# Kernel tuning notes

Hardware: AMD Instinct MI355X
Metric: run time of the kernel (lower is better)

The kernel has to match this reference:

```python
import jax, jax.numpy as jnp
import numpy as np

EPS = 1e-8


def setup_inputs() -> dict:
    key = jax.random.key(0)
    k1, k2, k3, k4 = jax.random.split(key, 4)
    N, E, d = 10000, 5000, 128
    F = jax.random.normal(k1, (N, d), dtype=jnp.float32)
    H = jax.random.uniform(k2, (N, E), dtype=jnp.float32)
    Dv = jax.random.uniform(k3, (N, N), dtype=jnp.float32)
    De = jax.random.uniform(k4, (E, E), dtype=jnp.float32)
    return {"F": F, "H": H, "Dv": Dv, "De": De}


def reference(F, H, Dv, De):
    # Only the diagonals of Dv/De are used by the original (torch.diag extraction).
    dv = jnp.diagonal(Dv)                      # [N]
    de = jnp.diagonal(De)                      # [E]
    dv_inv_sqrt = (dv + EPS) ** -0.5           # diag of Dv^{-1/2}
    de_inv = 1.0 / (de + EPS)                  # diag of De^{-1}
    # L = I - Dv^{-1/2} H De^{-1} H^T Dv^{-1/2}
    # trace(F^T L F) = ||F||_F^2 - sum_e de_inv[e] * ||(H^T (Dv^{-1/2} F))[e]||^2
    Fs = F * dv_inv_sqrt[:, None]              # [N, d]
    M = H.T @ Fs                               # [E, d]
    trace_term = jnp.sum(F * F) - jnp.sum(de_inv[:, None] * (M * M))
    # use_rayleigh=False; reduction='mean' -> divide by N
    loss = trace_term / F.shape[0]
    return loss
```

## Files before the change

### kernel.cpp

```cpp
#include <hip/hip_runtime.h>

#define EPSF 1e-8f

typedef __attribute__((ext_vector_type(8))) short bf16x8;
typedef __attribute__((ext_vector_type(4))) float f32x4;

constexpr int Nv     = 10000;
constexpr int Ne     = 5000;
constexpr int Dd     = 128;
constexpr int NPAD   = 10016;
constexpr int EPAD   = 5120;
constexpr int KSTEPS = 313;
constexpr int KSPLIT = 16;
constexpr int STEPS_PER = (KSTEPS + KSPLIT - 1) / KSPLIT;

__device__ __forceinline__ unsigned short f2bf_rne(float f) {
    unsigned int u = __builtin_bit_cast(unsigned int, f);
    u += 0x7fffu + ((u >> 16) & 1u);
    return (unsigned short)(u >> 16);
}

__global__ void prep_de_kernel(const float* __restrict__ De, float* __restrict__ de_inv) {
    int e = blockIdx.x * 256 + threadIdx.x;
    if (e < EPAD) de_inv[e] = (e < Ne) ? 1.0f / (De[(size_t)e * (Ne + 1)] + EPSF) : 0.0f;
}

__global__ void prep_fst_kernel(const float* __restrict__ F, const float* __restrict__ Dv,
                                short* __restrict__ Fst) {
    int n = blockIdx.x * 256 + threadIdx.x;
    int c = blockIdx.y;
    if (n < NPAD) {
        unsigned short b = 0;
        if (n < Nv) {
            float s = 1.0f / sqrtf(Dv[(size_t)n * (Nv + 1)] + EPSF);
            b = f2bf_rne(F[(size_t)n * Dd + c] * s);
        }
        Fst[(size_t)c * NPAD + n] = (short)b;
    }
}

__global__ void sum_ff_kernel(const float* __restrict__ F, float* __restrict__ out0) {
    const float4* F4 = (const float4*)F;
    int base = blockIdx.x * 512 + threadIdx.x;
    float4 a = F4[base];
    float4 b = F4[base + 256];
    float sum = a.x*a.x + a.y*a.y + a.z*a.z + a.w*a.w
              + b.x*b.x + b.y*b.y + b.z*b.z + b.w*b.w;
    #pragma unroll
    for (int off = 32; off; off >>= 1) sum += __shfl_down(sum, off);
    if ((threadIdx.x & 63) == 0) atomicAdd(out0, sum);
}

__global__ __launch_bounds__(256, 2)
void gemm_split_kernel(const float* __restrict__ H, const short* __restrict__ Fst,
                       float* __restrict__ M) {
    __shared__ unsigned int Alds[128 * 20];

    const int t  = threadIdx.x;
    const int w  = t >> 6;
    const int l  = t & 63;
    const int lm = l & 15;
    const int q  = l >> 4;
    const int e0 = blockIdx.x * 128;
    const int sb = blockIdx.y * STEPS_PER;
    const int se = min(sb + STEPS_PER, KSTEPS);

    const int rp  = t & 15;
    const int cp4 = t >> 4;

    f32x4 acc[2][8];
    #pragma unroll
    for (int a = 0; a < 2; ++a)
        #pragma unroll
        for (int b = 0; b < 8; ++b) acc[a][b] = (f32x4){0.f, 0.f, 0.f, 0.f};

    for (int s = sb; s < se; ++s) {
        const int n0 = s * 32;

        bf16x8 Bf[8];
        #pragma unroll
        for (int cb = 0; cb < 8; ++cb) {
            const int c = cb * 16 + lm;
            Bf[cb] = *(const bf16x8*)(Fst + (size_t)c * NPAD + n0 + q * 8);
        }

        const int n  = n0 + 2 * rp;
        const bool vn = (n < Nv);
        #pragma unroll
        for (int j = 0; j < 4; ++j) {
            const int cp = cp4 + 16 * j;
            const int el = 2 * cp;
            const int e  = e0 + el;
            float2 a0 = make_float2(0.f, 0.f), a1 = make_float2(0.f, 0.f);
            if (vn && e < Ne) {
                a0 = *(const float2*)(H + (size_t)n * Ne + e);
                a1 = *(const float2*)(H + (size_t)(n + 1) * Ne + e);
            }
            unsigned int w0 = (unsigned int)f2bf_rne(a0.x) | ((unsigned int)f2bf_rne(a1.x) << 16);
            unsigned int w1 = (unsigned int)f2bf_rne(a0.y) | ((unsigned int)f2bf_rne(a1.y) << 16);
            Alds[el * 20 + rp]       = w0;
            Alds[(el + 1) * 20 + rp] = w1;
        }
        __syncthreads();

        bf16x8 Af[2];
        #pragma unroll
        for (int eb = 0; eb < 2; ++eb) {
            const int el = (2 * w + eb) * 16 + lm;
            Af[eb] = *(const bf16x8*)((const char*)Alds + el * 80 + q * 16);
        }
        __syncthreads();

        #pragma unroll
        for (int cb = 0; cb < 8; ++cb)
            #pragma unroll
            for (int eb = 0; eb < 2; ++eb)
                acc[eb][cb] = __builtin_amdgcn_mfma_f32_16x16x32_bf16(
                    Af[eb], Bf[cb], acc[eb][cb], 0, 0, 0);
    }

    #pragma unroll
    for (int eb = 0; eb < 2; ++eb) {
        #pragma unroll
        for (int cb = 0; cb < 8; ++cb) {
            const int c = cb * 16 + lm;
            #pragma unroll
            for (int r = 0; r < 4; ++r) {
                const int el = (2 * w + eb) * 16 + q * 4 + r;
                atomicAdd(&M[(size_t)(e0 + el) * 128 + c], acc[eb][cb][r]);
            }
        }
    }
}

__global__ void reduce_m_kernel(const float* __restrict__ M, const float* __restrict__ de_inv,
                                float* __restrict__ outS) {
    const float4* M4 = (const float4*)M;
    int base = blockIdx.x * 512 + threadIdx.x;
    float sum = 0.f;
    #pragma unroll
    for (int i = 0; i < 2; ++i) {
        int idx = base + i * 256;
        float4 m = M4[idx];
        float wgt = de_inv[idx >> 5];
        sum += wgt * (m.x*m.x + m.y*m.y + m.z*m.z + m.w*m.w);
    }
    #pragma unroll
    for (int off = 32; off; off >>= 1) sum += __shfl_down(sum, off);
    if ((threadIdx.x & 63) == 0) atomicAdd(outS, sum);
}

__global__ void final_kernel(const float* __restrict__ ws0, float* __restrict__ out) {
    out[0] = (ws0[0] - ws0[1]) * (1.0f / (float)Nv);
}

extern "C" void kernel_launch(void* const* d_in, const int* in_sizes, int n_in,
                              void* d_out, int out_size, void* d_ws, size_t ws_size,
                              hipStream_t stream) {
    (void)in_sizes; (void)n_in; (void)out_size; (void)ws_size;
    const float* F  = (const float*)d_in[0];
    const float* H  = (const float*)d_in[1];
    const float* Dv = (const float*)d_in[2];
    const float* De = (const float*)d_in[3];
    float* out = (float*)d_out;

    float* ws0    = (float*)d_ws;
    float* M      = ws0 + 16;
    float* de_inv = M + (size_t)EPAD * 128;
    short* Fst    = (short*)(de_inv + EPAD);

    hipMemsetAsync(d_ws, 0, 64 + (size_t)EPAD * 128 * 4, stream);

    prep_de_kernel <<<EPAD / 256, 256, 0, stream>>>(De, de_inv);
    prep_fst_kernel<<<dim3((NPAD + 255) / 256, 128), 256, 0, stream>>>(F, Dv, Fst);
    sum_ff_kernel  <<<625, 256, 0, stream>>>(F, ws0);
    gemm_split_kernel<<<dim3(EPAD / 128, KSPLIT), 256, 0, stream>>>(H, Fst, M);
    reduce_m_kernel<<<320, 256, 0, stream>>>(M, de_inv, ws0 + 1);
    final_kernel   <<<1, 1, 0, stream>>>(ws0, out);
}
```

Measured before the change: 709.5 us.

## Restructure GEMM to per-wave 32x32 MFMA tiles with split-K partial buffers

The shared-memory-staged block GEMM is replaced by independent waves. Each wave owns a 32-column slice of H and accumulates all 128 feature columns with 32x32x16 bf16 MFMAs, reading H directly from global memory with a one-step register prefetch. The float atomics into M are replaced by plain stores into per-split partial buffers, which the reduce kernel sums and weights, so M no longer needs a large memset. The diagonal extraction is precomputed once and the sum of F squared is folded into the prep kernel. The per-lane H loads are strided by row (a single float per row), which risks poorer coalescing than before, and the partial buffers add extra memory traffic.

After: 964.3 us. +35.9%, slower.

```diff
diff --git a/kernel.cpp b/kernel.cpp
--- a/kernel.cpp
+++ b/kernel.cpp
@@ -3,16 +3,16 @@
 #define EPSF 1e-8f
 
 typedef __attribute__((ext_vector_type(8))) short bf16x8;
-typedef __attribute__((ext_vector_type(4))) float f32x4;
+typedef __attribute__((ext_vector_type(16))) float f32x16;
 
 constexpr int Nv     = 10000;
 constexpr int Ne     = 5000;
 constexpr int Dd     = 128;
 constexpr int NPAD   = 10016;
-constexpr int EPAD   = 5120;
-constexpr int KSTEPS = 313;
+constexpr int NT16   = 626;
+constexpr int ETILES = 157;
+constexpr int EW     = ETILES * 32;
 constexpr int KSPLIT = 16;
-constexpr int STEPS_PER = (KSTEPS + KSPLIT - 1) / KSPLIT;
 
 __device__ __forceinline__ unsigned short f2bf_rne(float f) {
     unsigned int u = __builtin_bit_cast(unsigned int, f);
@@ -20,131 +20,106 @@
     return (unsigned short)(u >> 16);
 }
 
-__global__ void prep_de_kernel(const float* __restrict__ De, float* __restrict__ de_inv) {
-    int e = blockIdx.x * 256 + threadIdx.x;
-    if (e < EPAD) de_inv[e] = (e < Ne) ? 1.0f / (De[(size_t)e * (Ne + 1)] + EPSF) : 0.0f;
+__global__ void prep_diag_kernel(const float* __restrict__ Dv, const float* __restrict__ De,
+                                 float* __restrict__ dvis, float* __restrict__ de_inv) {
+    int i = blockIdx.x * 256 + threadIdx.x;
+    if (i < NPAD) dvis[i] = (i < Nv) ? rsqrtf(Dv[(size_t)i * (Nv + 1)] + EPSF) : 0.0f;
+    if (i < EW)   de_inv[i] = (i < Ne) ? 1.0f / (De[(size_t)i * (Ne + 1)] + EPSF) : 0.0f;
 }
 
-__global__ void prep_fst_kernel(const float* __restrict__ F, const float* __restrict__ Dv,
-                                short* __restrict__ Fst) {
+__global__ void prep_fst_kernel(const float* __restrict__ F, const float* __restrict__ dvis,
+                                short* __restrict__ Fst, float* __restrict__ out0) {
     int n = blockIdx.x * 256 + threadIdx.x;
     int c = blockIdx.y;
+    float v = 0.0f;
     if (n < NPAD) {
         unsigned short b = 0;
-        if (n < Nv) {
-            float s = 1.0f / sqrtf(Dv[(size_t)n * (Nv + 1)] + EPSF);
-            b = f2bf_rne(F[(size_t)n * Dd + c] * s);
-        }
+        if (n < Nv) { v = F[(size_t)n * Dd + c]; b = f2bf_rne(v * dvis[n]); }
         Fst[(size_t)c * NPAD + n] = (short)b;
     }
-}
-
-__global__ void sum_ff_kernel(const float* __restrict__ F, float* __restrict__ out0) {
-    const float4* F4 = (const float4*)F;
-    int base = blockIdx.x * 512 + threadIdx.x;
-    float4 a = F4[base];
-    float4 b = F4[base + 256];
-    float sum = a.x*a.x + a.y*a.y + a.z*a.z + a.w*a.w
-              + b.x*b.x + b.y*b.y + b.z*b.z + b.w*b.w;
+    float sum = v * v;
     #pragma unroll
     for (int off = 32; off; off >>= 1) sum += __shfl_down(sum, off);
     if ((threadIdx.x & 63) == 0) atomicAdd(out0, sum);
 }
 
-__global__ __launch_bounds__(256, 2)
-void gemm_split_kernel(const float* __restrict__ H, const short* __restrict__ Fst,
-                       float* __restrict__ M) {
-    __shared__ unsigned int Alds[128 * 20];
+__global__ __launch_bounds__(256, 4)
+void gemm_kernel(const float* __restrict__ H, const short* __restrict__ Fst,
+                 float* __restrict__ Mp) {
+    const int t    = threadIdx.x;
+    const int w    = t >> 6;
+    const int l    = t & 63;
+    const int em   = l & 31;
+    const int half = l >> 5;
+    const int gw   = blockIdx.x * 4 + w;
+    const int et   = gw % ETILES;
+    const int spl  = gw / ETILES;
+    const int e    = et * 32 + em;
+    const bool ev  = (e < Ne);
+    const int sb   = (spl * NT16) / KSPLIT;
+    const int se   = ((spl + 1) * NT16) / KSPLIT;
 
-    const int t  = threadIdx.x;
-    const int w  = t >> 6;
-    const int l  = t & 63;
-    const int lm = l & 15;
-    const int q  = l >> 4;
-    const int e0 = blockIdx.x * 128;
-    const int sb = blockIdx.y * STEPS_PER;
-    const int se = min(sb + STEPS_PER, KSTEPS);
+    f32x16 acc[4];
+    #pragma unroll
+    for (int ct = 0; ct < 4; ++ct) acc[ct] = (f32x16)(0.0f);
 
-    const int rp  = t & 15;
-    const int cp4 = t >> 4;
+    float bc[8], bn[8];
+    auto loadB = [&](int s, float* b) {
+        const int kb = s * 16 + half * 8;
+        #pragma unroll
+        for (int j = 0; j < 8; ++j) {
+            const int n = kb + j;
+            b[j] = (ev && n < Nv) ? H[(size_t)n * Ne + e] : 0.0f;
+        }
+    };
 
-    f32x4 acc[2][8];
-    #pragma unroll
-    for (int a = 0; a < 2; ++a)
+    loadB(sb, bc);
+    for (int s = sb; s < se; ++s) {
         #pragma unroll
-        for (int b = 0; b < 8; ++b) acc[a][b] = (f32x4){0.f, 0.f, 0.f, 0.f};
+        for (int j = 0; j < 8; ++j) bn[j] = 0.0f;
+        if (s + 1 < se) loadB(s + 1, bn);
 
-    for (int s = sb; s < se; ++s) {
-        const int n0 = s * 32;
+        bf16x8 Bf;
+        #pragma unroll
+        for (int j = 0; j < 8; ++j) Bf[j] = (short)f2bf_rne(bc[j]);
 
-        bf16x8 Bf[8];
+        const int kb = s * 16 + half * 8;
+        bf16x8 Af[4];
         #pragma unroll
-        for (int cb = 0; cb < 8; ++cb) {
-            const int c = cb * 16 + lm;
-            Bf[cb] = *(const bf16x8*)(Fst + (size_t)c * NPAD + n0 + q * 8);
-        }
-
-        const int n  = n0 + 2 * rp;
-        const bool vn = (n < Nv);
-        #pragma unroll
-        for (int j = 0; j < 4; ++j) {
-            const int cp = cp4 + 16 * j;
-            const int el = 2 * cp;
-            const int e  = e0 + el;
-            float2 a0 = make_float2(0.f, 0.f), a1 = make_float2(0.f, 0.f);
-            if (vn && e < Ne) {
-                a0 = *(const float2*)(H + (size_t)n * Ne + e);
-                a1 = *(const float2*)(H + (size_t)(n + 1) * Ne + e);
-            }
-            unsigned int w0 = (unsigned int)f2bf_rne(a0.x) | ((unsigned int)f2bf_rne(a1.x) << 16);
-            unsigned int w1 = (unsigned int)f2bf_rne(a0.y) | ((unsigned int)f2bf_rne(a1.y) << 16);
-            Alds[el * 20 + rp]       = w0;
-            Alds[(el + 1) * 20 + rp] = w1;
-        }
-        __syncthreads();
-
-        bf16x8 Af[2];
-        #pragma unroll
-        for (int eb = 0; eb < 2; ++eb) {
-            const int el = (2 * w + eb) * 16 + lm;
-            Af[eb] = *(const bf16x8*)((const char*)Alds + el * 80 + q * 16);
-        }
-        __syncthreads();
+        for (int ct = 0; ct < 4; ++ct)
+            Af[ct] = *(const bf16x8*)(Fst + (size_t)(ct * 32 + em) * NPAD + kb);
 
         #pragma unroll
-        for (int cb = 0; cb < 8; ++cb)
-            #pragma unroll
-            for (int eb = 0; eb < 2; ++eb)
-                acc[eb][cb] = __builtin_amdgcn_mfma_f32_16x16x32_bf16(
-                    Af[eb], Bf[cb], acc[eb][cb], 0, 0, 0);
+        for (int ct = 0; ct < 4; ++ct)
+            acc[ct] = __builtin_amdgcn_mfma_f32_32x32x16_bf16(Af[ct], Bf, acc[ct], 0, 0, 0);
+
+        #pragma unroll
+        for (int j = 0; j < 8; ++j) bc[j] = bn[j];
     }
 
+    float* dst = Mp + (size_t)spl * 128 * EW;
     #pragma unroll
-    for (int eb = 0; eb < 2; ++eb) {
+    for (int ct = 0; ct < 4; ++ct)
         #pragma unroll
-        for (int cb = 0; cb < 8; ++cb) {
-            const int c = cb * 16 + lm;
-            #pragma unroll
-            for (int r = 0; r < 4; ++r) {
-                const int el = (2 * w + eb) * 16 + q * 4 + r;
-                atomicAdd(&M[(size_t)(e0 + el) * 128 + c], acc[eb][cb][r]);
-            }
+        for (int r = 0; r < 16; ++r) {
+            const int cl = (r & 3) + 8 * (r >> 2) + 4 * half;
+            dst[(size_t)(ct * 32 + cl) * EW + e] = acc[ct][r];
         }
-    }
 }
 
-__global__ void reduce_m_kernel(const float* __restrict__ M, const float* __restrict__ de_inv,
+__global__ void reduce_m_kernel(const float* __restrict__ Mp, const float* __restrict__ de_inv,
                                 float* __restrict__ outS) {
-    const float4* M4 = (const float4*)M;
-    int base = blockIdx.x * 512 + threadIdx.x;
-    float sum = 0.f;
+    int gid = blockIdx.x * 256 + threadIdx.x;
+    int c   = gid / (EW / 4);
+    int ei  = (gid % (EW / 4)) * 4;
+    float4 m = {0.f, 0.f, 0.f, 0.f};
     #pragma unroll
-    for (int i = 0; i < 2; ++i) {
-        int idx = base + i * 256;
-        float4 m = M4[idx];
-        float wgt = de_inv[idx >> 5];
-        sum += wgt * (m.x*m.x + m.y*m.y + m.z*m.z + m.w*m.w);
+    for (int sp = 0; sp < KSPLIT; ++sp) {
+        float4 p = *(const float4*)(Mp + ((size_t)sp * 128 + c) * EW + ei);
+        m.x += p.x; m.y += p.y; m.z += p.z; m.w += p.w;
     }
+    float4 w4 = *(const float4*)(de_inv + ei);
+    float sum = w4.x*m.x*m.x + w4.y*m.y*m.y + w4.z*m.z*m.z + w4.w*m.w*m.w;
     #pragma unroll
     for (int off = 32; off; off >>= 1) sum += __shfl_down(sum, off);
     if ((threadIdx.x & 63) == 0) atomicAdd(outS, sum);
@@ -165,16 +140,16 @@
     float* out = (float*)d_out;
 
     float* ws0    = (float*)d_ws;
-    float* M      = ws0 + 16;
-    float* de_inv = M + (size_t)EPAD * 128;
-    short* Fst    = (short*)(de_inv + EPAD);
+    float* dvis   = ws0 + 16;
+    float* de_inv = dvis + NPAD;
+    float* Mp     = de_inv + EW;
+    short* Fst    = (short*)(Mp + (size_t)KSPLIT * 128 * EW);
 
-    hipMemsetAsync(d_ws, 0, 64 + (size_t)EPAD * 128 * 4, stream);
+    hipMemsetAsync(ws0, 0, 64, stream);
 
-    prep_de_kernel <<<EPAD / 256, 256, 0, stream>>>(De, de_inv);
-    prep_fst_kernel<<<dim3((NPAD + 255) / 256, 128), 256, 0, stream>>>(F, Dv, Fst);
-    sum_ff_kernel  <<<625, 256, 0, stream>>>(F, ws0);
-    gemm_split_kernel<<<dim3(EPAD / 128, KSPLIT), 256, 0, stream>>>(H, Fst, M);
-    reduce_m_kernel<<<320, 256, 0, stream>>>(M, de_inv, ws0 + 1);
-    final_kernel   <<<1, 1, 0, stream>>>(ws0, out);
+    prep_diag_kernel<<<(NPAD + 255) / 256, 256, 0, stream>>>(Dv, De, dvis, de_inv);
+    prep_fst_kernel <<<dim3((NPAD + 255) / 256, 128), 256, 0, stream>>>(F, dvis, Fst, ws0);
+    gemm_kernel     <<<(ETILES * KSPLIT) / 4, 256, 0, stream>>>(H, Fst, Mp);
+    reduce_m_kernel <<<(128 * EW / 4) / 256, 256, 0, stream>>>(Mp, de_inv, ws0 + 1);
+    final_kernel    <<<1, 1, 0, stream>>>(ws0, out);
 }
```
